# Kernel optimization log

Hardware: AMD Instinct MI355X
Metric: run time of the kernel (lower is better)

The kernel has to match this reference:

```python
import jax, jax.numpy as jnp
import numpy as np

N_STACK = 32
ZERO_OFFSET = 1e-6
EPS = 1e-8
POW_EPS = 1e-12  # guard for 0**sharpen gradient


def _cos_sim(a, b):
    # a: [D] param, b: [B, D]; matches torch.cosine_similarity with eps=1e-8
    an = jnp.maximum(jnp.sqrt(jnp.sum(a * a)), EPS)
    bn = jnp.maximum(jnp.sqrt(jnp.sum(b * b, axis=-1)), EPS)
    return (b @ a) / (an * bn)


def _elu(x):
    return jnp.where(x > 0, x, jnp.expm1(x))


def setup_inputs() -> dict:
    key = jax.random.key(0)
    k0, k1, k2, k3 = jax.random.split(key, 4)
    B, T, D = 128, 256, 256
    return {
        "x": jax.random.normal(k0, (B, T, D), jnp.float32),
        "should_pop": jax.random.normal(k1, (D,), jnp.float32),
        "sharpen_pointer": jnp.array([5.0], jnp.float32),
        "latch_enable": jax.random.normal(k2, (D,), jnp.float32) * 0.01,
        "latch_init": jax.random.normal(k3, (B, D), jnp.float32),
    }


def _forward(x, should_pop, sharpen_pointer, latch_enable, latch_init):
    B, T, D = x.shape
    dtype = x.dtype
    stack0 = jnp.full((B, N_STACK, D), ZERO_OFFSET, dtype)
    ptr0 = jnp.full((B, N_STACK), ZERO_OFFSET, dtype).at[:, 0].set(1.0)
    sharpen = sharpen_pointer[0]

    def step(carry, inp):
        stack, ptr, latch = carry  # [B,N,D], [B,N], [B,D]
        # pop gate from PREVIOUS latch state (relay of length 1)
        pop = _elu(_cos_sim(should_pop, latch))            # [B]
        push = 1.0 - pop
        # push branch: advance pointer, write value at new slot
        p_push = jnp.roll(ptr, 1, axis=1)
        st_push = stack * (1.0 - p_push)[..., None] + inp[:, None, :] * p_push[..., None]
        # pop branch: erase current slot to zero_offset, retreat pointer
        st_pop = stack * (1.0 - ptr)[..., None] + ZERO_OFFSET * ptr[..., None]
        p_pop = jnp.roll(ptr, -1, axis=1)
        # superpose push/pop (null_op weight is exactly 0 in this module)
        new_stack = push[:, None, None] * st_push + pop[:, None, None] * st_pop
        new_ptr = push[:, None] * p_push + pop[:, None] * p_pop
        # sharpen pointer: relu, pow, renormalize
        p = jnp.maximum(jax.nn.relu(new_ptr), POW_EPS) ** sharpen
        p = p / jnp.maximum(jnp.sum(p, axis=1, keepdims=True), EPS)
        # read and gate output
        s = jnp.einsum('bnv,bn->bv', new_stack, p)
        out = pop[:, None] * s
        # latch update: gate = elu(cos(enable_param, inp)); dropout is eval-mode no-op
        g = _elu(_cos_sim(latch_enable, inp))
        new_latch = g[:, None] * inp + (1.0 - g)[:, None] * latch
        return (new_stack, p, new_latch), out

    _, outs = jax.lax.scan(step, (stack0, ptr0, latch_init), jnp.swapaxes(x, 0, 1))
    return jnp.swapaxes(outs, 0, 1)  # [B, T, D]


def reference(x, should_pop, sharpen_pointer, latch_enable, latch_init):
    return _forward(x, should_pop, sharpen_pointer, latch_enable, latch_init)
```

## Files before the change

kernel.cpp:

```cpp
#include <hip/hip_runtime.h>
#include <math.h>


#define NSTK 32
#define DDIM 256
#define ZO 1e-6f
#define EPSC 1e-8f
#define PEPS 1e-12f
#define TTILE 32
#define MAXT 1024

__device__ __forceinline__ float elu_f(float c) {
    return (c > 0.f) ? c : expm1f(c);
}

__device__ __forceinline__ float dpp_xor1(float x) {
    return __int_as_float(__builtin_amdgcn_update_dpp(0, __float_as_int(x), 0xB1, 0xF, 0xF, true));
}
__device__ __forceinline__ float dpp_xor2(float x) {
    return __int_as_float(__builtin_amdgcn_update_dpp(0, __float_as_int(x), 0x4E, 0xF, 0xF, true));
}
__device__ __forceinline__ float dpp_halfmirror(float x) {
    return __int_as_float(__builtin_amdgcn_update_dpp(0, __float_as_int(x), 0x141, 0xF, 0xF, true));
}
__device__ __forceinline__ float dpp_mirror(float x) {
    return __int_as_float(__builtin_amdgcn_update_dpp(0, __float_as_int(x), 0x140, 0xF, 0xF, true));
}
__device__ __forceinline__ float swz_xor16(float x) {
    return __int_as_float(__builtin_amdgcn_ds_swizzle(__float_as_int(x), 0x401F));
}

__global__ void gate4_kernel(const float* __restrict__ vecs,
                             const float* __restrict__ par,
                             float* __restrict__ gout,
                             int T) {
    const int b = blockIdx.y;
    const int t = blockIdx.x * 4 + (threadIdx.x >> 6);
    const int lane = threadIdx.x & 63;
    const float4 v = *(const float4*)(vecs + ((size_t)b * T + t) * DDIM + lane * 4);
    const float4 p = *(const float4*)(par + lane * 4);
    float r0 = v.x * p.x + v.y * p.y + v.z * p.z + v.w * p.w;
    float r1 = v.x * v.x + v.y * v.y + v.z * v.z + v.w * v.w;
    float r2 = p.x * p.x + p.y * p.y + p.z * p.z + p.w * p.w;
#pragma unroll
    for (int off = 32; off >= 1; off >>= 1) {
        r0 += __shfl_xor(r0, off, 64);
        r1 += __shfl_xor(r1, off, 64);
        r2 += __shfl_xor(r2, off, 64);
    }
    if (lane == 0) {
        const float c = r0 / (fmaxf(sqrtf(r2), EPSC) * fmaxf(sqrtf(r1), EPSC));
        gout[(size_t)b * T + t] = elu_f(c);
    }
}

__global__ void latch_scan_kernel(const float* __restrict__ x,
                                  const float* __restrict__ latch0,
                                  const float* __restrict__ g,
                                  float* __restrict__ L,
                                  int T) {
    const int b = blockIdx.x >> 2;
    const int dt = blockIdx.x & 3;
    const int d = dt * 64 + threadIdx.x;
    const float* xb = x + (size_t)b * T * DDIM + d;
    const float* gb = g + (size_t)b * T;
    float* Lb = L + (size_t)b * T * DDIM + d;
    float l = latch0[(size_t)b * DDIM + d];
    for (int c = 0; c < T; c += 32) {
        float xv[32], gv[32];
#pragma unroll
        for (int i = 0; i < 32; i++) xv[i] = xb[(size_t)(c + i) * DDIM];
#pragma unroll
        for (int i = 0; i < 32; i++) gv[i] = gb[c + i];
#pragma unroll
        for (int i = 0; i < 32; i++) {
            Lb[(size_t)(c + i) * DDIM] = l;
            l = fmaf(gv[i], xv[i] - l, l);
        }
    }
}

__launch_bounds__(64, 1)
__global__ void ptr_scan_kernel(const float* __restrict__ pop_arr,
                                const float* __restrict__ sharpen_ptr,
                                float* __restrict__ scal,
                                int T) {
    const int b0 = blockIdx.x * 2;
    const int tid = threadIdx.x;
    const int n = tid & 31;
    const int grp = tid >> 5;
    const float sharpen = sharpen_ptr[0];
    const bool sharp5 = (sharpen == 5.0f);

    __shared__ float pops[2 * MAXT];
    for (int i = tid; i < 2 * T; i += 64) pops[i] = pop_arr[(size_t)b0 * T + i];
    __syncthreads();
    const float* popg = pops + grp * T;

    float* scb = scal + (size_t)(b0 + grp) * T * 128;

    float u = (n == 0) ? 1.0f : ZO;
    float invu = 1.0f;

#pragma unroll 2
    for (int t = 0; t < T; t++) {
        const float pop = popg[t];
        const float push = 1.0f - pop;
        const float up = __shfl(u, (n + 31) & 31, 32);
        const float un = __shfl(u, (n + 1) & 31, 32);
        const float r = fmaf(push, up, pop * un);
        const float np = r * invu;
        const float q = fmaxf(np, PEPS);
        float unew;
        if (sharp5) { const float q2 = q * q, q4 = q2 * q2; unew = q4 * q; }
        else        { unew = exp2f(sharpen * log2f(q)); }
        float s = unew;
        s += dpp_xor1(s);
        s += dpp_xor2(s);
        s += dpp_halfmirror(s);
        s += dpp_mirror(s);
        s += swz_xor16(s);
        const float invn = 1.0f / fmaxf(s, EPSC);
        const float p = u * invu;
        const float ppn = up * invu;
        const float pnew = unew * invn;
        float* row = scb + (size_t)t * 128;
        row[n]      = fmaf(push, -ppn, push) + fmaf(pop, -p, pop);
        row[32 + n] = push * ppn;
        row[64 + n] = pop * p * ZO;
        row[96 + n] = pop * pnew;
        u = unew; invu = invn;
    }
}

__launch_bounds__(256, 2)
__global__ void stack_kernel(const float* __restrict__ x,
                             const float* __restrict__ scal,
                             float* __restrict__ out,
                             int T) {
    const int b = blockIdx.y;
    const int dtile = blockIdx.x;
    const int tid = threadIdx.x;
    const int wave = tid >> 6;
    const int lane = tid & 63;
    const int dsub = lane & 15;
    const int ng = lane >> 4;

    __shared__ float sc_s[2][TTILE * 128];
    __shared__ float x_s[2][TTILE * 64];

    const float* scb = scal + (size_t)b * T * 128;
    const float* xtb = x + (size_t)b * T * DDIM + dtile * 64;
    float* ob = out + (size_t)b * T * DDIM + dtile * 64 + wave * 16 + dsub;

    const int f0 = tid, f1 = tid + 256;
    const int tr0 = f0 >> 4, dq0 = (f0 & 15) * 4;
    const int tr1 = f1 >> 4, dq1 = (f1 & 15) * 4;

    float4 sreg[4], xreg[2];

    auto load_tile = [&](int t0) {
        const float4* sg = (const float4*)(scb + (size_t)t0 * 128);
        sreg[0] = sg[tid];
        sreg[1] = sg[tid + 256];
        sreg[2] = sg[tid + 512];
        sreg[3] = sg[tid + 768];
        xreg[0] = *(const float4*)(xtb + (size_t)(t0 + tr0) * DDIM + dq0);
        xreg[1] = *(const float4*)(xtb + (size_t)(t0 + tr1) * DDIM + dq1);
    };
    auto store_tile = [&](int buf) {
        float4* ss = (float4*)sc_s[buf];
        ss[tid] = sreg[0];
        ss[tid + 256] = sreg[1];
        ss[tid + 512] = sreg[2];
        ss[tid + 768] = sreg[3];
        float4* xs = (float4*)x_s[buf];
        xs[f0] = xreg[0];
        xs[f1] = xreg[1];
    };

    float st[8];
#pragma unroll
    for (int j = 0; j < 8; j++) st[j] = ZO;

    load_tile(0);
    store_tile(0);
    __syncthreads();

    const int NT = T / TTILE;
    for (int tile = 0; tile < NT; tile++) {
        if (tile + 1 < NT) load_tile((tile + 1) * TTILE);
        const float* scl = sc_s[tile & 1];
        const float* xl = x_s[tile & 1] + wave * 16 + dsub;
        const int tglob = tile * TTILE;
#pragma unroll 4
        for (int tl = 0; tl < TTILE; tl++) {
            const float4* sc4 = (const float4*)(scl + tl * 128) + ng * 2;
            const float4 a0 = sc4[0],  a1 = sc4[1];
            const float4 b0 = sc4[8],  b1 = sc4[9];
            const float4 g0 = sc4[16], g1 = sc4[17];
            const float4 w0 = sc4[24], w1 = sc4[25];
            const float xv = xl[tl * 64];

            float acc;
            st[0] = fmaf(a0.x, st[0], fmaf(b0.x, xv, g0.x)); acc  = st[0] * w0.x;
            st[1] = fmaf(a0.y, st[1], fmaf(b0.y, xv, g0.y)); acc += st[1] * w0.y;
            st[2] = fmaf(a0.z, st[2], fmaf(b0.z, xv, g0.z)); acc += st[2] * w0.z;
            st[3] = fmaf(a0.w, st[3], fmaf(b0.w, xv, g0.w)); acc += st[3] * w0.w;
            st[4] = fmaf(a1.x, st[4], fmaf(b1.x, xv, g1.x)); acc += st[4] * w1.x;
            st[5] = fmaf(a1.y, st[5], fmaf(b1.y, xv, g1.y)); acc += st[5] * w1.y;
            st[6] = fmaf(a1.z, st[6], fmaf(b1.z, xv, g1.z)); acc += st[6] * w1.z;
            st[7] = fmaf(a1.w, st[7], fmaf(b1.w, xv, g1.w)); acc += st[7] * w1.w;

            acc += __shfl_xor(acc, 16, 64);
            acc += __shfl_xor(acc, 32, 64);
            if (ng == 0) ob[(size_t)(tglob + tl) * DDIM] = acc;
        }
        if (tile + 1 < NT) store_tile((tile + 1) & 1);
        __syncthreads();
    }
}

__launch_bounds__(256, 1)
__global__ void neuralstack_kernel(const float* __restrict__ x,
                                   const float* __restrict__ should_pop,
                                   const float* __restrict__ sharpen_ptr,
                                   const float* __restrict__ latch_enable,
                                   const float* __restrict__ latch_init,
                                   float* __restrict__ out,
                                   int T) {
    const int b = blockIdx.x;
    const int tid = threadIdx.x;
    const int wave = tid >> 6;
    const int lane = tid & 63;
    __shared__ float red[2][16];
    const float sp_d = should_pop[tid];
    const float le_d = latch_enable[tid];
    const float sharpen = sharpen_ptr[0];
    float latch = latch_init[(size_t)b * DDIM + tid];
    float a0 = sp_d * sp_d, a1 = le_d * le_d;
#pragma unroll
    for (int off = 32; off >= 1; off >>= 1) {
        a0 += __shfl_xor(a0, off, 64);
        a1 += __shfl_xor(a1, off, 64);
    }
    if (lane == 0) { red[0][wave * 4] = a0; red[0][wave * 4 + 1] = a1; }
    __syncthreads();
    const float an_sp = fmaxf(sqrtf(red[0][0] + red[0][4] + red[0][8] + red[0][12]), EPSC);
    const float an_le = fmaxf(sqrtf(red[0][1] + red[0][5] + red[0][9] + red[0][13]), EPSC);
    __syncthreads();
    float st[NSTK], ptr[NSTK];
#pragma unroll
    for (int n = 0; n < NSTK; n++) { st[n] = ZO; ptr[n] = (n == 0) ? 1.0f : ZO; }
    const float* xb = x + (size_t)b * T * DDIM + tid;
    float* ob = out + (size_t)b * T * DDIM + tid;
    const bool sharp5 = (sharpen == 5.0f);
    float inp = xb[0];
    for (int t = 0; t < T; t++) {
        const int tn = (t + 1 < T) ? (t + 1) : (T - 1);
        const float inp_next = xb[(size_t)tn * DDIM];
        float r0 = sp_d * latch, r1 = latch * latch, r2 = le_d * inp, r3 = inp * inp;
#pragma unroll
        for (int off = 32; off >= 1; off >>= 1) {
            r0 += __shfl_xor(r0, off, 64);
            r1 += __shfl_xor(r1, off, 64);
            r2 += __shfl_xor(r2, off, 64);
            r3 += __shfl_xor(r3, off, 64);
        }
        const int buf = t & 1;
        if (lane == 0) {
            red[buf][wave * 4] = r0; red[buf][wave * 4 + 1] = r1;
            red[buf][wave * 4 + 2] = r2; red[buf][wave * 4 + 3] = r3;
        }
        __syncthreads();
        const float s0 = red[buf][0] + red[buf][4] + red[buf][8] + red[buf][12];
        const float s1 = red[buf][1] + red[buf][5] + red[buf][9] + red[buf][13];
        const float s2 = red[buf][2] + red[buf][6] + red[buf][10] + red[buf][14];
        const float s3 = red[buf][3] + red[buf][7] + red[buf][11] + red[buf][15];
        const float pop = elu_f(s0 / (an_sp * fmaxf(sqrtf(s1), EPSC)));
        const float push = 1.0f - pop;
        const float g = elu_f(s2 / (an_le * fmaxf(sqrtf(s3), EPSC)));
        float q[NSTK];
#pragma unroll
        for (int n = 0; n < NSTK; n++) {
            const float pp = ptr[(n + NSTK - 1) & (NSTK - 1)];
            const float pn = ptr[(n + 1) & (NSTK - 1)];
            q[n] = fmaxf(push * pp + pop * pn, PEPS);
        }
        if (sharp5) {
#pragma unroll
            for (int n = 0; n < NSTK; n++) { const float v = q[n], v2 = v * v; q[n] = v2 * v2 * v; }
        } else {
#pragma unroll
            for (int n = 0; n < NSTK; n++) q[n] = exp2f(sharpen * log2f(q[n]));
        }
        float qa = 0.f, qb = 0.f, qc = 0.f, qd = 0.f;
#pragma unroll
        for (int n = 0; n < NSTK; n += 4) { qa += q[n]; qb += q[n+1]; qc += q[n+2]; qd += q[n+3]; }
        const float inv = 1.0f / fmaxf((qa + qb) + (qc + qd), EPSC);
        float sacc = 0.f;
#pragma unroll
        for (int n = 0; n < NSTK; n++) {
            const float pp = ptr[(n + NSTK - 1) & (NSTK - 1)];
            const float pc = ptr[n];
            const float ns = push * (st[n] + pp * (inp - st[n])) + pop * (st[n] + pc * (ZO - st[n]));
            st[n] = ns;
            sacc += ns * (q[n] * inv);
        }
#pragma unroll
        for (int n = 0; n < NSTK; n++) ptr[n] = q[n] * inv;
        ob[(size_t)t * DDIM] = pop * sacc;
        latch = fmaf(g, inp - latch, latch);
        inp = inp_next;
    }
}

extern "C" void kernel_launch(void* const* d_in, const int* in_sizes, int n_in,
                              void* d_out, int out_size, void* d_ws, size_t ws_size,
                              hipStream_t stream) {
    const float* x = (const float*)d_in[0];
    const float* should_pop = (const float*)d_in[1];
    const float* sharpen_ptr = (const float*)d_in[2];
    const float* latch_enable = (const float*)d_in[3];
    const float* latch_init = (const float*)d_in[4];
    float* out = (float*)d_out;

    const int D = in_sizes[1];
    const int B = in_sizes[4] / D;
    const int T = in_sizes[0] / in_sizes[4];
    (void)n_in; (void)out_size;

    const size_t BT = (size_t)B * T;
    const size_t off_g = 0;
    const size_t off_pop = BT;
    const size_t off_L = 2 * BT;
    const size_t off_scal = off_L + BT * D;
    const size_t need_floats = off_scal + BT * 128;

    if (ws_size < need_floats * sizeof(float) || D != DDIM ||
        (T % TTILE) != 0 || (T % 4) != 0 || (B % 2) != 0 || T > MAXT) {
        neuralstack_kernel<<<B, 256, 0, stream>>>(x, should_pop, sharpen_ptr,
                                                  latch_enable, latch_init, out, T);
        return;
    }

    float* ws = (float*)d_ws;
    float* g = ws + off_g;
    float* pop = ws + off_pop;
    float* L = ws + off_L;
    float* scal = ws + off_scal;

    gate4_kernel<<<dim3(T / 4, B), 256, 0, stream>>>(x, latch_enable, g, T);
    latch_scan_kernel<<<B * 4, 64, 0, stream>>>(x, latch_init, g, L, T);
    gate4_kernel<<<dim3(T / 4, B), 256, 0, stream>>>(L, should_pop, pop, T);
    ptr_scan_kernel<<<B / 2, 64, 0, stream>>>(pop, sharpen_ptr, scal, T);
    stack_kernel<<<dim3(D / 64, B), 256, 0, stream>>>(x, scal, out, T);
}
```

Baseline: 227.3 us.

## Store only normalized pointers and recompute stack coefficients inside the stack kernel

The pointer scan now writes just the 32 normalized pointer weights per step instead of 128 precomputed coefficients. The stack kernel rebuilds the push/pop/erase coefficients on the fly from the current and previous pointer, the pop value and a cross-lane shuffle for the rolled slot. The stack kernel also moves to single-wave blocks over 16-column tiles, with a single LDS buffer and no block barriers. The pointer scan prefetches pop values in float4 chunks. This cuts the intermediate workspace traffic in exchange for extra ALU work per step and more, smaller blocks.

After: 224.7 us. Within noise of the previous version (-1.1%).

```diff
diff --git a/kernel.cpp b/kernel.cpp
--- a/kernel.cpp
+++ b/kernel.cpp
@@ -83,7 +83,7 @@
 __launch_bounds__(64, 1)
 __global__ void ptr_scan_kernel(const float* __restrict__ pop_arr,
                                 const float* __restrict__ sharpen_ptr,
-                                float* __restrict__ scal,
+                                float* __restrict__ Parr,
                                 int T) {
     const int b0 = blockIdx.x * 2;
     const int tid = threadIdx.x;
@@ -96,21 +96,18 @@
     for (int i = tid; i < 2 * T; i += 64) pops[i] = pop_arr[(size_t)b0 * T + i];
     __syncthreads();
     const float* popg = pops + grp * T;
-
-    float* scb = scal + (size_t)(b0 + grp) * T * 128;
+    float* Pb = Parr + (size_t)(b0 + grp) * T * 32;
 
     float u = (n == 0) ? 1.0f : ZO;
     float invu = 1.0f;
-
-#pragma unroll 2
-    for (int t = 0; t < T; t++) {
-        const float pop = popg[t];
+    int t = 0;
+
+    auto step = [&](float pop) {
         const float push = 1.0f - pop;
         const float up = __shfl(u, (n + 31) & 31, 32);
         const float un = __shfl(u, (n + 1) & 31, 32);
         const float r = fmaf(push, up, pop * un);
-        const float np = r * invu;
-        const float q = fmaxf(np, PEPS);
+        const float q = fmaxf(r * invu, PEPS);
         float unew;
         if (sharp5) { const float q2 = q * q, q4 = q2 * q2; unew = q4 * q; }
         else        { unew = exp2f(sharpen * log2f(q)); }
@@ -121,103 +118,116 @@
         s += dpp_mirror(s);
         s += swz_xor16(s);
         const float invn = 1.0f / fmaxf(s, EPSC);
-        const float p = u * invu;
-        const float ppn = up * invu;
-        const float pnew = unew * invn;
-        float* row = scb + (size_t)t * 128;
-        row[n]      = fmaf(push, -ppn, push) + fmaf(pop, -p, pop);
-        row[32 + n] = push * ppn;
-        row[64 + n] = pop * p * ZO;
-        row[96 + n] = pop * pnew;
+        Pb[(size_t)t * 32 + n] = unew * invn;
         u = unew; invu = invn;
-    }
-}
-
-__launch_bounds__(256, 2)
+        t++;
+    };
+
+    const float4* p4 = (const float4*)popg;
+    float4 cA0 = p4[0], cA1 = p4[1], cA2 = p4[2], cA3 = p4[3];
+    for (int c = 0; c < T; c += 16) {
+        float4 cB0, cB1, cB2, cB3;
+        if (c + 16 < T) {
+            const float4* pn4 = p4 + (c + 16) / 4;
+            cB0 = pn4[0]; cB1 = pn4[1]; cB2 = pn4[2]; cB3 = pn4[3];
+        }
+        step(cA0.x); step(cA0.y); step(cA0.z); step(cA0.w);
+        step(cA1.x); step(cA1.y); step(cA1.z); step(cA1.w);
+        step(cA2.x); step(cA2.y); step(cA2.z); step(cA2.w);
+        step(cA3.x); step(cA3.y); step(cA3.z); step(cA3.w);
+        if (c + 16 < T) { cA0 = cB0; cA1 = cB1; cA2 = cB2; cA3 = cB3; }
+    }
+}
+
+__launch_bounds__(64, 1)
 __global__ void stack_kernel(const float* __restrict__ x,
-                             const float* __restrict__ scal,
+                             const float* __restrict__ Parr,
+                             const float* __restrict__ pop_arr,
                              float* __restrict__ out,
                              int T) {
     const int b = blockIdx.y;
     const int dtile = blockIdx.x;
-    const int tid = threadIdx.x;
-    const int wave = tid >> 6;
-    const int lane = tid & 63;
+    const int lane = threadIdx.x;
     const int dsub = lane & 15;
     const int ng = lane >> 4;
 
-    __shared__ float sc_s[2][TTILE * 128];
-    __shared__ float x_s[2][TTILE * 64];
-
-    const float* scb = scal + (size_t)b * T * 128;
-    const float* xtb = x + (size_t)b * T * DDIM + dtile * 64;
-    float* ob = out + (size_t)b * T * DDIM + dtile * 64 + wave * 16 + dsub;
-
-    const int f0 = tid, f1 = tid + 256;
-    const int tr0 = f0 >> 4, dq0 = (f0 & 15) * 4;
-    const int tr1 = f1 >> 4, dq1 = (f1 & 15) * 4;
-
-    float4 sreg[4], xreg[2];
-
-    auto load_tile = [&](int t0) {
-        const float4* sg = (const float4*)(scb + (size_t)t0 * 128);
-        sreg[0] = sg[tid];
-        sreg[1] = sg[tid + 256];
-        sreg[2] = sg[tid + 512];
-        sreg[3] = sg[tid + 768];
-        xreg[0] = *(const float4*)(xtb + (size_t)(t0 + tr0) * DDIM + dq0);
-        xreg[1] = *(const float4*)(xtb + (size_t)(t0 + tr1) * DDIM + dq1);
+    __shared__ float Ps[TTILE * 32];
+    __shared__ float xs[TTILE * 16];
+    __shared__ float ps[TTILE];
+
+    const float* Pb = Parr + (size_t)b * T * 32;
+    const float* xtb = x + (size_t)b * T * DDIM + dtile * 16;
+    const float* popb = pop_arr + (size_t)b * T;
+    float* ob = out + (size_t)b * T * DDIM + dtile * 16 + dsub;
+
+    float4 Preg0, Preg1, Preg2, Preg3, xreg0, xreg1, popreg;
+    const int f0 = lane, f1 = lane + 64;
+    const int xr0 = f0 >> 2, xc0 = (f0 & 3) * 4;
+    const int xr1 = f1 >> 2, xc1 = (f1 & 3) * 4;
+
+    auto load_regs = [&](int t0) {
+        const float4* P4 = (const float4*)(Pb + (size_t)t0 * 32);
+        Preg0 = P4[lane];
+        Preg1 = P4[lane + 64];
+        Preg2 = P4[lane + 128];
+        Preg3 = P4[lane + 192];
+        xreg0 = *(const float4*)(xtb + (size_t)(t0 + xr0) * DDIM + xc0);
+        xreg1 = *(const float4*)(xtb + (size_t)(t0 + xr1) * DDIM + xc1);
+        if (lane < 8) popreg = *(const float4*)(popb + t0 + lane * 4);
     };
-    auto store_tile = [&](int buf) {
-        float4* ss = (float4*)sc_s[buf];
-        ss[tid] = sreg[0];
-        ss[tid + 256] = sreg[1];
-        ss[tid + 512] = sreg[2];
-        ss[tid + 768] = sreg[3];
-        float4* xs = (float4*)x_s[buf];
-        xs[f0] = xreg[0];
-        xs[f1] = xreg[1];
+    auto store_lds = [&]() {
+        ((float4*)Ps)[lane] = Preg0;
+        ((float4*)Ps)[lane + 64] = Preg1;
+        ((float4*)Ps)[lane + 128] = Preg2;
+        ((float4*)Ps)[lane + 192] = Preg3;
+        ((float4*)xs)[f0] = xreg0;
+        ((float4*)xs)[f1] = xreg1;
+        if (lane < 8) ((float4*)ps)[lane] = popreg;
     };
 
-    float st[8];
-#pragma unroll
-    for (int j = 0; j < 8; j++) st[j] = ZO;
-
-    load_tile(0);
-    store_tile(0);
-    __syncthreads();
+    float st[8], pc[8];
+#pragma unroll
+    for (int i = 0; i < 8; i++) { st[i] = ZO; pc[i] = ZO; }
+    if (ng == 0) pc[0] = 1.0f;
+
+    load_regs(0);
+    store_lds();
 
     const int NT = T / TTILE;
     for (int tile = 0; tile < NT; tile++) {
-        if (tile + 1 < NT) load_tile((tile + 1) * TTILE);
-        const float* scl = sc_s[tile & 1];
-        const float* xl = x_s[tile & 1] + wave * 16 + dsub;
-        const int tglob = tile * TTILE;
+        if (tile + 1 < NT) load_regs((tile + 1) * TTILE);
+        const int tg0 = tile * TTILE;
 #pragma unroll 4
         for (int tl = 0; tl < TTILE; tl++) {
-            const float4* sc4 = (const float4*)(scl + tl * 128) + ng * 2;
-            const float4 a0 = sc4[0],  a1 = sc4[1];
-            const float4 b0 = sc4[8],  b1 = sc4[9];
-            const float4 g0 = sc4[16], g1 = sc4[17];
-            const float4 w0 = sc4[24], w1 = sc4[25];
-            const float xv = xl[tl * 64];
-
-            float acc;
-            st[0] = fmaf(a0.x, st[0], fmaf(b0.x, xv, g0.x)); acc  = st[0] * w0.x;
-            st[1] = fmaf(a0.y, st[1], fmaf(b0.y, xv, g0.y)); acc += st[1] * w0.y;
-            st[2] = fmaf(a0.z, st[2], fmaf(b0.z, xv, g0.z)); acc += st[2] * w0.z;
-            st[3] = fmaf(a0.w, st[3], fmaf(b0.w, xv, g0.w)); acc += st[3] * w0.w;
-            st[4] = fmaf(a1.x, st[4], fmaf(b1.x, xv, g1.x)); acc += st[4] * w1.x;
-            st[5] = fmaf(a1.y, st[5], fmaf(b1.y, xv, g1.y)); acc += st[5] * w1.y;
-            st[6] = fmaf(a1.z, st[6], fmaf(b1.z, xv, g1.z)); acc += st[6] * w1.z;
-            st[7] = fmaf(a1.w, st[7], fmaf(b1.w, xv, g1.w)); acc += st[7] * w1.w;
-
+            const float pop = ps[tl];
+            const float push = 1.0f - pop;
+            const float4 pn0 = *(const float4*)(Ps + tl * 32 + ng * 8);
+            const float4 pn1 = *(const float4*)(Ps + tl * 32 + ng * 8 + 4);
+            const float xv = xs[tl * 16 + dsub];
+            const float pm1 = __shfl(pc[7], ((ng + 3) & 3) * 16 + dsub, 64);
+            const float pn[8] = {pn0.x, pn0.y, pn0.z, pn0.w,
+                                 pn1.x, pn1.y, pn1.z, pn1.w};
+            float acc = 0.f;
+#pragma unroll
+            for (int i = 0; i < 8; i++) {
+                const float p_s = pc[i];
+                const float pp_s = (i == 0) ? pm1 : pc[i - 1];
+                const float t0v = pop * p_s;
+                const float m = fmaf(push, pp_s, t0v);
+                const float alpha = 1.0f - m;
+                const float beta = push * pp_s;
+                const float bxg = fmaf(beta, xv, ZO * t0v);
+                const float ns = fmaf(alpha, st[i], bxg);
+                st[i] = ns;
+                acc = fmaf(pn[i], ns, acc);
+            }
+#pragma unroll
+            for (int i = 0; i < 8; i++) pc[i] = pn[i];
             acc += __shfl_xor(acc, 16, 64);
             acc += __shfl_xor(acc, 32, 64);
-            if (ng == 0) ob[(size_t)(tglob + tl) * DDIM] = acc;
-        }
-        if (tile + 1 < NT) store_tile((tile + 1) & 1);
-        __syncthreads();
+            if (ng == 0) ob[(size_t)(tg0 + tl) * DDIM] = pop * acc;
+        }
+        if (tile + 1 < NT) store_lds();
     }
 }
 
@@ -302,8 +312,8 @@
 #pragma unroll
         for (int n = 0; n < NSTK; n++) {
             const float pp = ptr[(n + NSTK - 1) & (NSTK - 1)];
-            const float pc = ptr[n];
-            const float ns = push * (st[n] + pp * (inp - st[n])) + pop * (st[n] + pc * (ZO - st[n]));
+            const float pc_ = ptr[n];
+            const float ns = push * (st[n] + pp * (inp - st[n])) + pop * (st[n] + pc_ * (ZO - st[n]));
             st[n] = ns;
             sacc += ns * (q[n] * inv);
         }
@@ -334,11 +344,11 @@
     const size_t off_g = 0;
     const size_t off_pop = BT;
     const size_t off_L = 2 * BT;
-    const size_t off_scal = off_L + BT * D;
-    const size_t need_floats = off_scal + BT * 128;
+    const size_t off_P = off_L + BT * D;
+    const size_t need_floats = off_P + BT * 32;
 
     if (ws_size < need_floats * sizeof(float) || D != DDIM ||
-        (T % TTILE) != 0 || (T % 4) != 0 || (B % 2) != 0 || T > MAXT) {
+        (T % TTILE) != 0 || (B % 2) != 0 || T > MAXT) {
         neuralstack_kernel<<<B, 256, 0, stream>>>(x, should_pop, sharpen_ptr,
                                                   latch_enable, latch_init, out, T);
         return;
@@ -348,11 +358,11 @@
     float* g = ws + off_g;
     float* pop = ws + off_pop;
     float* L = ws + off_L;
-    float* scal = ws + off_scal;
+    float* P = ws + off_P;
 
     gate4_kernel<<<dim3(T / 4, B), 256, 0, stream>>>(x, latch_enable, g, T);
     latch_scan_kernel<<<B * 4, 64, 0, stream>>>(x, latch_init, g, L, T);
     gate4_kernel<<<dim3(T / 4, B), 256, 0, stream>>>(L, should_pop, pop, T);
-    ptr_scan_kernel<<<B / 2, 64, 0, stream>>>(pop, sharpen_ptr, scal, T);
-    stack_kernel<<<dim3(D / 64, B), 256, 0, stream>>>(x, scal, out, T);
-}
+    ptr_scan_kernel<<<B / 2, 64, 0, stream>>>(pop, sharpen_ptr, P, T);
+    stack_kernel<<<dim3(D / 16, B), 64, 0, stream>>>(x, P, pop, out, T);
+}
```
